# Kernel tuning notes

Measured on AMD Instinct MI355X. Metric: run time of the kernel, lower is better.

## Reference

```python
import jax, jax.numpy as jnp
import numpy as np
from jax import lax

B, N, M = 2, 16384, 4096
C1, C2 = 128, 256
H1, H2 = 256, 128  # mlp = [C1+C2, 256, 128]


def setup_inputs() -> dict:
    key = jax.random.key(0)
    ks = jax.random.split(key, 8)
    return {
        "unknown": jax.random.normal(ks[0], (B, N, 3), jnp.float32),
        "known": jax.random.normal(ks[1], (B, M, 3), jnp.float32),
        "unknow_feats": jax.random.normal(ks[2], (B, C1, N), jnp.float32),
        "known_feats": jax.random.normal(ks[3], (B, C2, M), jnp.float32),
        "W1": jax.random.normal(ks[4], (H1, C1 + C2), jnp.float32) * 0.05,
        "b1": jnp.zeros((H1,), jnp.float32),
        "W2": jax.random.normal(ks[5], (H2, H1), jnp.float32) * 0.05,
        "b2": jnp.zeros((H2,), jnp.float32),
    }


def reference(unknown, known, unknow_feats, known_feats, W1, b1, W2, b2):
    # Pairwise squared distances (B, n, m) via ||a||^2 + ||b||^2 - 2 a.b
    d2 = (
        jnp.sum(unknown * unknown, -1)[:, :, None]
        + jnp.sum(known * known, -1)[:, None, :]
        - 2.0 * jnp.einsum("bnd,bmd->bnm", unknown, known)
    )
    # 3 nearest neighbors
    neg_d2, idx = lax.top_k(-d2, 3)  # (B, n, 3)
    dist = jnp.sqrt(jnp.maximum(-neg_d2, 0.0))  # pointops returns sqrt distances
    dist_recip = 1.0 / (dist + 1e-8)
    weight = dist_recip / jnp.sum(dist_recip, axis=2, keepdims=True)  # (B, n, 3)
    # Gather neighbor features (B, C2, n, 3) and inverse-distance weighted sum
    gathered = jax.vmap(lambda f, i: f[:, i])(known_feats, idx)
    interpolated = jnp.sum(gathered * weight[:, None, :, :], axis=-1)  # (B, C2, n)
    new_features = jnp.concatenate([interpolated, unknow_feats], axis=1)  # (B, C1+C2, n)
    # Shared MLP (1x1 convs, bn=False -> conv bias + ReLU)
    h = jax.nn.relu(jnp.einsum("oc,bcn->bon", W1, new_features) + b1[None, :, None])
    out = jax.nn.relu(jnp.einsum("oc,bcn->bon", W2, h) + b2[None, :, None])
    return out  # (B, mlp[-1], n)
```

## Files before the change

### kernel.cpp

```cpp
#include <hip/hip_runtime.h>
#include <hip/hip_bf16.h>

#define BB 2
#define NN 16384
#define MM 4096
#define C1 128
#define C2 256
#define CIN 384
#define H1 256
#define H2 128
#define PT 32
#define XROW 392

typedef __attribute__((ext_vector_type(8))) short bf16x8;
typedef __attribute__((ext_vector_type(4))) float f32x4;
typedef __attribute__((ext_vector_type(2))) float f32x2;
typedef __attribute__((ext_vector_type(8))) float f32x8;

__device__ __forceinline__ short f32_to_bf16(float x) {
    unsigned u = __float_as_uint(x);
    u += 0x7fffu + ((u >> 16) & 1u);
    return (short)(u >> 16);
}
__device__ __forceinline__ float bf16_to_f32(unsigned short u) {
    union { unsigned u; float f; } c; c.u = ((unsigned)u) << 16; return c.f;
}
__device__ __forceinline__ unsigned pack_bf16x2(float a, float b) {
    __hip_bfloat162 h = __float22bfloat162_rn(make_float2(a, b));
    union { __hip_bfloat162 h; unsigned u; } cv;
    cv.h = h;
    return cv.u;
}

__global__ __launch_bounds__(1024) void kpk_prep_kernel(
    const float* __restrict__ known, float* __restrict__ kpk8)
{
    int i = blockIdx.x * 1024 + threadIdx.x;
    if (i < BB * MM) {
        float x = known[3 * i + 0], y = known[3 * i + 1], z = known[3 * i + 2];
        float n = fmaf(x, x, fmaf(y, y, z * z));
        int g = i >> 1, j = i & 1;
        float* base = kpk8 + (size_t)g * 8;
        base[0 + j] = x; base[2 + j] = y; base[4 + j] = z; base[6 + j] = n;
    }
}

__global__ __launch_bounds__(1024) void knn_aux_kernel(
    const float* __restrict__ unknown,
    const float* __restrict__ kpk8,
    int*   __restrict__ idx_out,
    float* __restrict__ w_out,
    const float* __restrict__ KF,
    unsigned short* __restrict__ KT16,
    const float* __restrict__ W1, const float* __restrict__ W2,
    short* __restrict__ W1b, short* __restrict__ W2b)
{
    __shared__ float pdv[16][64][3];
    __shared__ float vf[64];
    __shared__ float msc[64][8];
    __shared__ int   mid[64][8];
    __shared__ int   cnt[64];
    __shared__ float tl[32][33];

    const int bx  = blockIdx.x;
    const int tid = threadIdx.x;

    if (bx < 512) {
        const int lane = tid & 63;
        const int wv   = __builtin_amdgcn_readfirstlane(tid >> 6);
        const int b    = bx >> 8;
        const int n    = (bx & 255) * 64 + lane;

        if (tid < 64) cnt[tid] = 0;

        const float ux = unknown[((size_t)b * NN + n) * 3 + 0];
        const float uy = unknown[((size_t)b * NN + n) * 3 + 1];
        const float uz = unknown[((size_t)b * NN + n) * 3 + 2];
        const f32x2 ax2 = {-2.f * ux, -2.f * ux};
        const f32x2 ay2 = {-2.f * uy, -2.f * uy};
        const f32x2 az2 = {-2.f * uz, -2.f * uz};
        const float un = fmaf(ux, ux, fmaf(uy, uy, uz * uz));

        const int gbase = wv * 128;
        const float* __restrict__ kp = kpk8 + ((size_t)b * (MM / 2) + gbase) * 8;

        float v0 = 3e38f, v1 = 3e38f, v2 = 3e38f;
        #pragma unroll 4
        for (int g = 0; g < 128; ++g) {
            const f32x8 G = *(const f32x8*)(kp + (size_t)g * 8);
            const f32x2 kx = __builtin_shufflevector(G, G, 0, 1);
            const f32x2 ky = __builtin_shufflevector(G, G, 2, 3);
            const f32x2 kz = __builtin_shufflevector(G, G, 4, 5);
            const f32x2 kn = __builtin_shufflevector(G, G, 6, 7);
            const f32x2 sc2 = __builtin_elementwise_fma(ax2, kx,
                              __builtin_elementwise_fma(ay2, ky,
                              __builtin_elementwise_fma(az2, kz, kn)));
            float sa = sc2.x;
            v2 = __builtin_amdgcn_fmed3f(v1, sa, v2);
            v1 = __builtin_amdgcn_fmed3f(v0, sa, v1);
            v0 = fminf(sa, v0);
            float sb = sc2.y;
            v2 = __builtin_amdgcn_fmed3f(v1, sb, v2);
            v1 = __builtin_amdgcn_fmed3f(v0, sb, v1);
            v0 = fminf(sb, v0);
        }
        pdv[wv][lane][0] = v0; pdv[wv][lane][1] = v1; pdv[wv][lane][2] = v2;
        __syncthreads();

        if (tid < 64) {
            float r0 = 3e38f, r1 = 3e38f, r2 = 3e38f;
            #pragma unroll
            for (int ww = 0; ww < 16; ++ww) {
                #pragma unroll
                for (int k = 0; k < 3; ++k) {
                    float d = pdv[ww][tid][k];
                    r2 = __builtin_amdgcn_fmed3f(r1, d, r2);
                    r1 = __builtin_amdgcn_fmed3f(r0, d, r1);
                    r0 = fminf(d, r0);
                }
            }
            vf[tid] = r2;
        }
        __syncthreads();

        const float v2f = vf[lane];
        #pragma unroll 4
        for (int g = 0; g < 128; ++g) {
            const f32x8 G = *(const f32x8*)(kp + (size_t)g * 8);
            const f32x2 kx = __builtin_shufflevector(G, G, 0, 1);
            const f32x2 ky = __builtin_shufflevector(G, G, 2, 3);
            const f32x2 kz = __builtin_shufflevector(G, G, 4, 5);
            const f32x2 kn = __builtin_shufflevector(G, G, 6, 7);
            const f32x2 sc2 = __builtin_elementwise_fma(ax2, kx,
                              __builtin_elementwise_fma(ay2, ky,
                              __builtin_elementwise_fma(az2, kz, kn)));
            if (fminf(sc2.x, sc2.y) <= v2f) {
                if (sc2.x <= v2f) {
                    int c = atomicAdd(&cnt[lane], 1);
                    if (c < 8) { msc[lane][c] = sc2.x; mid[lane][c] = (gbase + g) * 2; }
                }
                if (sc2.y <= v2f) {
                    int c = atomicAdd(&cnt[lane], 1);
                    if (c < 8) { msc[lane][c] = sc2.y; mid[lane][c] = (gbase + g) * 2 + 1; }
                }
            }
        }
        __syncthreads();

        if (tid < 64) {
            const int c = cnt[tid] < 8 ? cnt[tid] : 8;
            float r0 = 3e38f, r1 = 3e38f, r2 = 3e38f;
            int   q0 = 0x7FFFFFFF, q1 = 0x7FFFFFFF, q2 = 0x7FFFFFFF;
            #pragma unroll
            for (int k = 0; k < 8; ++k) {
                float d = (k < c) ? msc[tid][k] : 3e38f;
                int   j = (k < c) ? mid[tid][k] : 0x7FFFFFFF;
                const bool lt0 = (d < r0) || (d == r0 && j < q0);
                const bool lt1 = (d < r1) || (d == r1 && j < q1);
                const bool lt2 = (d < r2) || (d == r2 && j < q2);
                float nr2 = lt1 ? r1 : (lt2 ? d : r2);
                int   nq2 = lt1 ? q1 : (lt2 ? j : q2);
                float nr1 = lt0 ? r0 : (lt1 ? d : r1);
                int   nq1 = lt0 ? q0 : (lt1 ? j : q1);
                float nr0 = lt0 ? d : r0;
                int   nq0 = lt0 ? j : q0;
                r0 = nr0; r1 = nr1; r2 = nr2; q0 = nq0; q1 = nq1; q2 = nq2;
            }
            float d0 = sqrtf(fmaxf(r0 + un, 0.f));
            float d1 = sqrtf(fmaxf(r1 + un, 0.f));
            float d2 = sqrtf(fmaxf(r2 + un, 0.f));
            float i0 = 1.f / (d0 + 1e-8f);
            float i1 = 1.f / (d1 + 1e-8f);
            float i2 = 1.f / (d2 + 1e-8f);
            float s  = i0 + i1 + i2;
            const size_t ob = ((size_t)(bx >> 8) * NN + n) * 3;
            idx_out[ob + 0] = q0; idx_out[ob + 1] = q1; idx_out[ob + 2] = q2;
            w_out[ob + 0] = i0 / s; w_out[ob + 1] = i1 / s; w_out[ob + 2] = i2 / s;
        }
    } else if (bx < 2560) {
        const int t  = bx - 512;
        const int b  = t >> 10;
        const int c0 = ((t >> 7) & 7) * 32;
        const int m0 = (t & 127) * 32;
        if (tid < 1024) {
            const int tx = tid & 31;
            const int ty = tid >> 5;
            tl[ty][tx] = KF[((size_t)b * C2 + c0 + ty) * MM + m0 + tx];
            __syncthreads();
            KT16[((size_t)b * MM + m0 + ty) * C2 + c0 + tx] = (unsigned short)f32_to_bf16(tl[tx][ty]);
        }
    } else {
        int i = (bx - 2560) * 1024 + tid;
        if (i < H1 * CIN) W1b[i] = f32_to_bf16(W1[i]);
        if (i < H2 * H1)  W2b[i] = f32_to_bf16(W2[i]);
    }
}

__global__ __launch_bounds__(256, 4) void fp_mlp_mfma_kernel(
    const float* __restrict__ unknow_feats,
    const unsigned short* __restrict__ KT16,
    const short* __restrict__ W1b,
    const float* __restrict__ b1,
    const short* __restrict__ W2b,
    const float* __restrict__ b2,
    const int*   __restrict__ idx,
    const float* __restrict__ wgt,
    float* __restrict__ out)
{
    __shared__ short XH[PT][XROW];
    __shared__ int   Is[PT * 3];
    __shared__ float Ws[PT * 3];

    const int tid  = threadIdx.x;
    const int blocks_per_b = NN / PT;
    const int b    = blockIdx.x / blocks_per_b;
    const int n0   = (blockIdx.x % blocks_per_b) * PT;
    const int w    = tid >> 6;
    const int lane = tid & 63;
    const int lr   = lane & 15;
    const int lq   = lane >> 4;

    if (tid < PT * 3) {
        const size_t base = ((size_t)b * NN + n0) * 3;
        Is[tid] = idx[base + tid];
        Ws[tid] = wgt[base + tid];
    }
    __syncthreads();

    {
        const unsigned short* KTb = KT16 + (size_t)b * MM * C2;
        const int c4 = (lane << 2);
        ushort4 g[8][3];
        #pragma unroll
        for (int i = 0; i < 8; ++i) {
            const int p = i * 4 + w;
            g[i][0] = *(const ushort4*)(KTb + (size_t)Is[3 * p + 0] * C2 + c4);
            g[i][1] = *(const ushort4*)(KTb + (size_t)Is[3 * p + 1] * C2 + c4);
            g[i][2] = *(const ushort4*)(KTb + (size_t)Is[3 * p + 2] * C2 + c4);
        }
        #pragma unroll
        for (int i = 0; i < 8; ++i) {
            const int p = i * 4 + w;
            const float w0 = Ws[3 * p + 0], w1 = Ws[3 * p + 1], w2 = Ws[3 * p + 2];
            float vx = fmaf(w0, bf16_to_f32(g[i][0].x), fmaf(w1, bf16_to_f32(g[i][1].x), w2 * bf16_to_f32(g[i][2].x)));
            float vy = fmaf(w0, bf16_to_f32(g[i][0].y), fmaf(w1, bf16_to_f32(g[i][1].y), w2 * bf16_to_f32(g[i][2].y)));
            float vz = fmaf(w0, bf16_to_f32(g[i][0].z), fmaf(w1, bf16_to_f32(g[i][1].z), w2 * bf16_to_f32(g[i][2].z)));
            float vw = fmaf(w0, bf16_to_f32(g[i][0].w), fmaf(w1, bf16_to_f32(g[i][1].w), w2 * bf16_to_f32(g[i][2].w)));
            uint2 pk;
            pk.x = pack_bf16x2(vx, vy);
            pk.y = pack_bf16x2(vz, vw);
            *(uint2*)&XH[p][c4] = pk;
        }
        const float* UFb = unknow_feats + (size_t)b * C1 * NN + n0;
        #pragma unroll
        for (int i = 0; i < 4; ++i) {
            int e  = i * 256 + tid;
            int cc = e >> 3;
            int nq = (e & 7) << 2;
            const float4 f = *(const float4*)(UFb + (size_t)cc * NN + nq);
            XH[nq + 0][C2 + cc] = f32_to_bf16(f.x);
            XH[nq + 1][C2 + cc] = f32_to_bf16(f.y);
            XH[nq + 2][C2 + cc] = f32_to_bf16(f.z);
            XH[nq + 3][C2 + cc] = f32_to_bf16(f.w);
        }
    }
    __syncthreads();

    f32x4 acc[4][2];
    #pragma unroll
    for (int t = 0; t < 4; ++t)
        #pragma unroll
        for (int p = 0; p < 2; ++p) acc[t][p] = (f32x4){0.f, 0.f, 0.f, 0.f};

    #pragma unroll 4
    for (int k0 = 0; k0 < CIN; k0 += 32) {
        bf16x8 a[4], x[2];
        #pragma unroll
        for (int t = 0; t < 4; ++t)
            a[t] = *(const bf16x8*)(W1b + (size_t)(w * 64 + t * 16 + lr) * CIN + k0 + lq * 8);
        #pragma unroll
        for (int p = 0; p < 2; ++p)
            x[p] = *(bf16x8*)&XH[p * 16 + lr][k0 + lq * 8];
        #pragma unroll
        for (int t = 0; t < 4; ++t)
            #pragma unroll
            for (int p = 0; p < 2; ++p)
                acc[t][p] = __builtin_amdgcn_mfma_f32_16x16x32_bf16(a[t], x[p], acc[t][p], 0, 0, 0);
    }
    __syncthreads();

    #pragma unroll
    for (int t = 0; t < 4; ++t) {
        const int obase = w * 64 + t * 16 + lq * 4;
        float bb0 = b1[obase + 0], bb1 = b1[obase + 1],
              bb2 = b1[obase + 2], bb3 = b1[obase + 3];
        #pragma unroll
        for (int p = 0; p < 2; ++p) {
            uint2 pk;
            pk.x = pack_bf16x2(fmaxf(acc[t][p].x + bb0, 0.f),
                               fmaxf(acc[t][p].y + bb1, 0.f));
            pk.y = pack_bf16x2(fmaxf(acc[t][p].z + bb2, 0.f),
                               fmaxf(acc[t][p].w + bb3, 0.f));
            *(uint2*)&XH[p * 16 + lr][obase] = pk;
        }
    }
    __syncthreads();

    {
        f32x4 acc2[2][2];
        #pragma unroll
        for (int t = 0; t < 2; ++t)
            #pragma unroll
            for (int p = 0; p < 2; ++p) acc2[t][p] = (f32x4){0.f, 0.f, 0.f, 0.f};

        #pragma unroll 4
        for (int k0 = 0; k0 < H1; k0 += 32) {
            bf16x8 a[2], h[2];
            #pragma unroll
            for (int t = 0; t < 2; ++t)
                a[t] = *(const bf16x8*)(W2b + (size_t)(w * 32 + t * 16 + lr) * H1 + k0 + lq * 8);
            #pragma unroll
            for (int p = 0; p < 2; ++p)
                h[p] = *(bf16x8*)&XH[p * 16 + lr][k0 + lq * 8];
            #pragma unroll
            for (int t = 0; t < 2; ++t)
                #pragma unroll
                for (int p = 0; p < 2; ++p)
                    acc2[t][p] = __builtin_amdgcn_mfma_f32_16x16x32_bf16(a[t], h[p], acc2[t][p], 0, 0, 0);
        }
        #pragma unroll
        for (int t = 0; t < 2; ++t) {
            const int obase = w * 32 + t * 16 + lq * 4;
            #pragma unroll
            for (int p = 0; p < 2; ++p) {
                const int n = n0 + p * 16 + lr;
                #pragma unroll
                for (int r = 0; r < 4; ++r) {
                    const int o = obase + r;
                    out[((size_t)b * H2 + o) * NN + n] =
                        fmaxf(((const float*)&acc2[t][p])[r] + b2[o], 0.f);
                }
            }
        }
    }
}

extern "C" void kernel_launch(void* const* d_in, const int* in_sizes, int n_in,
                              void* d_out, int out_size, void* d_ws, size_t ws_size,
                              hipStream_t stream) {
    const float* unknown      = (const float*)d_in[0];
    const float* known        = (const float*)d_in[1];
    const float* unknow_feats = (const float*)d_in[2];
    const float* known_feats  = (const float*)d_in[3];
    const float* W1           = (const float*)d_in[4];
    const float* b1           = (const float*)d_in[5];
    const float* W2           = (const float*)d_in[6];
    const float* b2           = (const float*)d_in[7];
    float* out = (float*)d_out;

    char* ws = (char*)d_ws;
    int*            idx  = (int*)(ws);
    float*          wgt  = (float*)(ws + 393216);
    short*          W1b  = (short*)(ws + 786432);
    short*          W2b  = (short*)(ws + 983040);
    float*          kpk8 = (float*)(ws + 1048576);
    unsigned short* KT16 = (unsigned short*)(ws + 1179648);

    kpk_prep_kernel<<<8, 1024, 0, stream>>>(known, kpk8);

    knn_aux_kernel<<<2656, 1024, 0, stream>>>(
        unknown, kpk8, idx, wgt, known_feats, KT16, W1, W2, W1b, W2b);

    fp_mlp_mfma_kernel<<<BB * (NN / PT), 256, 0, stream>>>(
        unknow_feats, KT16, W1b, b1, W2b, b2, idx, wgt, out);
}
```

Baseline: 166.2 us.

## Halve MLP point tile to 16, raise occupancy, split top-3 chains

Result: slower. 202.0 us (+21.5%).

```diff
diff --git a/kernel.cpp b/kernel.cpp
--- a/kernel.cpp
+++ b/kernel.cpp
@@ -9,7 +9,7 @@
 #define CIN 384
 #define H1 256
 #define H2 128
-#define PT 32
+#define PT 16
 #define XROW 392
 
 typedef __attribute__((ext_vector_type(8))) short bf16x8;
@@ -84,7 +84,8 @@
         const int gbase = wv * 128;
         const float* __restrict__ kp = kpk8 + ((size_t)b * (MM / 2) + gbase) * 8;
 
-        float v0 = 3e38f, v1 = 3e38f, v2 = 3e38f;
+        float va0 = 3e38f, va1 = 3e38f, va2 = 3e38f;
+        float vb0 = 3e38f, vb1 = 3e38f, vb2 = 3e38f;
         #pragma unroll 4
         for (int g = 0; g < 128; ++g) {
             const f32x8 G = *(const f32x8*)(kp + (size_t)g * 8);
@@ -96,15 +97,25 @@
                               __builtin_elementwise_fma(ay2, ky,
                               __builtin_elementwise_fma(az2, kz, kn)));
             float sa = sc2.x;
-            v2 = __builtin_amdgcn_fmed3f(v1, sa, v2);
-            v1 = __builtin_amdgcn_fmed3f(v0, sa, v1);
-            v0 = fminf(sa, v0);
+            va2 = __builtin_amdgcn_fmed3f(va1, sa, va2);
+            va1 = __builtin_amdgcn_fmed3f(va0, sa, va1);
+            va0 = fminf(sa, va0);
             float sb = sc2.y;
-            v2 = __builtin_amdgcn_fmed3f(v1, sb, v2);
-            v1 = __builtin_amdgcn_fmed3f(v0, sb, v1);
-            v0 = fminf(sb, v0);
-        }
-        pdv[wv][lane][0] = v0; pdv[wv][lane][1] = v1; pdv[wv][lane][2] = v2;
+            vb2 = __builtin_amdgcn_fmed3f(vb1, sb, vb2);
+            vb1 = __builtin_amdgcn_fmed3f(vb0, sb, vb1);
+            vb0 = fminf(sb, vb0);
+        }
+        {
+            float bv[3] = {vb0, vb1, vb2};
+            #pragma unroll
+            for (int k = 0; k < 3; ++k) {
+                float d = bv[k];
+                va2 = __builtin_amdgcn_fmed3f(va1, d, va2);
+                va1 = __builtin_amdgcn_fmed3f(va0, d, va1);
+                va0 = fminf(d, va0);
+            }
+        }
+        pdv[wv][lane][0] = va0; pdv[wv][lane][1] = va1; pdv[wv][lane][2] = va2;
         __syncthreads();
 
         if (tid < 64) {
@@ -182,7 +193,7 @@
         const int b  = t >> 10;
         const int c0 = ((t >> 7) & 7) * 32;
         const int m0 = (t & 127) * 32;
-        if (tid < 1024) {
+        {
             const int tx = tid & 31;
             const int ty = tid >> 5;
             tl[ty][tx] = KF[((size_t)b * C2 + c0 + ty) * MM + m0 + tx];
@@ -196,7 +207,7 @@
     }
 }
 
-__global__ __launch_bounds__(256, 4) void fp_mlp_mfma_kernel(
+__global__ __launch_bounds__(256, 7) void fp_mlp_mfma_kernel(
     const float* __restrict__ unknow_feats,
     const unsigned short* __restrict__ KT16,
     const short* __restrict__ W1b,
@@ -230,16 +241,16 @@
     {
         const unsigned short* KTb = KT16 + (size_t)b * MM * C2;
         const int c4 = (lane << 2);
-        ushort4 g[8][3];
-        #pragma unroll
-        for (int i = 0; i < 8; ++i) {
+        ushort4 g[4][3];
+        #pragma unroll
+        for (int i = 0; i < 4; ++i) {
             const int p = i * 4 + w;
             g[i][0] = *(const ushort4*)(KTb + (size_t)Is[3 * p + 0] * C2 + c4);
             g[i][1] = *(const ushort4*)(KTb + (size_t)Is[3 * p + 1] * C2 + c4);
             g[i][2] = *(const ushort4*)(KTb + (size_t)Is[3 * p + 2] * C2 + c4);
         }
         #pragma unroll
-        for (int i = 0; i < 8; ++i) {
+        for (int i = 0; i < 4; ++i) {
             const int p = i * 4 + w;
             const float w0 = Ws[3 * p + 0], w1 = Ws[3 * p + 1], w2 = Ws[3 * p + 2];
             float vx = fmaf(w0, bf16_to_f32(g[i][0].x), fmaf(w1, bf16_to_f32(g[i][1].x), w2 * bf16_to_f32(g[i][2].x)));
@@ -253,10 +264,10 @@
         }
         const float* UFb = unknow_feats + (size_t)b * C1 * NN + n0;
         #pragma unroll
-        for (int i = 0; i < 4; ++i) {
+        for (int i = 0; i < 2; ++i) {
             int e  = i * 256 + tid;
-            int cc = e >> 3;
-            int nq = (e & 7) << 2;
+            int cc = e >> 2;
+            int nq = (e & 3) << 2;
             const float4 f = *(const float4*)(UFb + (size_t)cc * NN + nq);
             XH[nq + 0][C2 + cc] = f32_to_bf16(f.x);
             XH[nq + 1][C2 + cc] = f32_to_bf16(f.y);
@@ -266,26 +277,20 @@
     }
     __syncthreads();
 
-    f32x4 acc[4][2];
+    f32x4 acc[4];
     #pragma unroll
-    for (int t = 0; t < 4; ++t)
-        #pragma unroll
-        for (int p = 0; p < 2; ++p) acc[t][p] = (f32x4){0.f, 0.f, 0.f, 0.f};
+    for (int t = 0; t < 4; ++t) acc[t] = (f32x4){0.f, 0.f, 0.f, 0.f};
 
     #pragma unroll 4
     for (int k0 = 0; k0 < CIN; k0 += 32) {
-        bf16x8 a[4], x[2];
+        bf16x8 a[4], x;
         #pragma unroll
         for (int t = 0; t < 4; ++t)
             a[t] = *(const bf16x8*)(W1b + (size_t)(w * 64 + t * 16 + lr) * CIN + k0 + lq * 8);
-        #pragma unroll
-        for (int p = 0; p < 2; ++p)
-            x[p] = *(bf16x8*)&XH[p * 16 + lr][k0 + lq * 8];
+        x = *(bf16x8*)&XH[lr][k0 + lq * 8];
         #pragma unroll
         for (int t = 0; t < 4; ++t)
-            #pragma unroll
-            for (int p = 0; p < 2; ++p)
-                acc[t][p] = __builtin_amdgcn_mfma_f32_16x16x32_bf16(a[t], x[p], acc[t][p], 0, 0, 0);
+            acc[t] = __builtin_amdgcn_mfma_f32_16x16x32_bf16(a[t], x, acc[t], 0, 0, 0);
     }
     __syncthreads();
 
@@ -294,52 +299,40 @@
         const int obase = w * 64 + t * 16 + lq * 4;
         float bb0 = b1[obase + 0], bb1 = b1[obase + 1],
               bb2 = b1[obase + 2], bb3 = b1[obase + 3];
-        #pragma unroll
-        for (int p = 0; p < 2; ++p) {
-            uint2 pk;
-            pk.x = pack_bf16x2(fmaxf(acc[t][p].x + bb0, 0.f),
-                               fmaxf(acc[t][p].y + bb1, 0.f));
-            pk.y = pack_bf16x2(fmaxf(acc[t][p].z + bb2, 0.f),
-                               fmaxf(acc[t][p].w + bb3, 0.f));
-            *(uint2*)&XH[p * 16 + lr][obase] = pk;
-        }
+        uint2 pk;
+        pk.x = pack_bf16x2(fmaxf(acc[t].x + bb0, 0.f),
+                           fmaxf(acc[t].y + bb1, 0.f));
+        pk.y = pack_bf16x2(fmaxf(acc[t].z + bb2, 0.f),
+                           fmaxf(acc[t].w + bb3, 0.f));
+        *(uint2*)&XH[lr][obase] = pk;
     }
     __syncthreads();
 
     {
-        f32x4 acc2[2][2];
-        #pragma unroll
-        for (int t = 0; t < 2; ++t)
-            #pragma unroll
-            for (int p = 0; p < 2; ++p) acc2[t][p] = (f32x4){0.f, 0.f, 0.f, 0.f};
+        f32x4 acc2[2];
+        #pragma unroll
+        for (int t = 0; t < 2; ++t) acc2[t] = (f32x4){0.f, 0.f, 0.f, 0.f};
 
         #pragma unroll 4
         for (int k0 = 0; k0 < H1; k0 += 32) {
-            bf16x8 a[2], h[2];
+            bf16x8 a[2], h;
             #pragma unroll
             for (int t = 0; t < 2; ++t)
                 a[t] = *(const bf16x8*)(W2b + (size_t)(w * 32 + t * 16 + lr) * H1 + k0 + lq * 8);
-            #pragma unroll
-            for (int p = 0; p < 2; ++p)
-                h[p] = *(bf16x8*)&XH[p * 16 + lr][k0 + lq * 8];
+            h = *(bf16x8*)&XH[lr][k0 + lq * 8];
             #pragma unroll
             for (int t = 0; t < 2; ++t)
-                #pragma unroll
-                for (int p = 0; p < 2; ++p)
-                    acc2[t][p] = __builtin_amdgcn_mfma_f32_16x16x32_bf16(a[t], h[p], acc2[t][p], 0, 0, 0);
+                acc2[t] = __builtin_amdgcn_mfma_f32_16x16x32_bf16(a[t], h, acc2[t], 0, 0, 0);
         }
         #pragma unroll
         for (int t = 0; t < 2; ++t) {
             const int obase = w * 32 + t * 16 + lq * 4;
-            #pragma unroll
-            for (int p = 0; p < 2; ++p) {
-                const int n = n0 + p * 16 + lr;
-                #pragma unroll
-                for (int r = 0; r < 4; ++r) {
-                    const int o = obase + r;
-                    out[((size_t)b * H2 + o) * NN + n] =
-                        fmaxf(((const float*)&acc2[t][p])[r] + b2[o], 0.f);
-                }
+            const int n = n0 + lr;
+            #pragma unroll
+            for (int r = 0; r < 4; ++r) {
+                const int o = obase + r;
+                out[((size_t)b * H2 + o) * NN + n] =
+                    fmaxf(((const float*)&acc2[t])[r] + b2[o], 0.f);
             }
         }
     }
```

## Process two point tiles per MLP block with prefetched gathers; split kNN chains

Applied to the files above, without the earlier changes.

New measurement: 167.9 us. Within noise of the previous version (+1.0%).

```diff
diff --git a/kernel.cpp b/kernel.cpp
--- a/kernel.cpp
+++ b/kernel.cpp
@@ -10,6 +10,7 @@
 #define H1 256
 #define H2 128
 #define PT 32
+#define TILES 2
 #define XROW 392
 
 typedef __attribute__((ext_vector_type(8))) short bf16x8;
@@ -84,7 +85,8 @@
         const int gbase = wv * 128;
         const float* __restrict__ kp = kpk8 + ((size_t)b * (MM / 2) + gbase) * 8;
 
-        float v0 = 3e38f, v1 = 3e38f, v2 = 3e38f;
+        float va0 = 3e38f, va1 = 3e38f, va2 = 3e38f;
+        float vb0 = 3e38f, vb1 = 3e38f, vb2 = 3e38f;
         #pragma unroll 4
         for (int g = 0; g < 128; ++g) {
             const f32x8 G = *(const f32x8*)(kp + (size_t)g * 8);
@@ -96,15 +98,25 @@
                               __builtin_elementwise_fma(ay2, ky,
                               __builtin_elementwise_fma(az2, kz, kn)));
             float sa = sc2.x;
-            v2 = __builtin_amdgcn_fmed3f(v1, sa, v2);
-            v1 = __builtin_amdgcn_fmed3f(v0, sa, v1);
-            v0 = fminf(sa, v0);
+            va2 = __builtin_amdgcn_fmed3f(va1, sa, va2);
+            va1 = __builtin_amdgcn_fmed3f(va0, sa, va1);
+            va0 = fminf(sa, va0);
             float sb = sc2.y;
-            v2 = __builtin_amdgcn_fmed3f(v1, sb, v2);
-            v1 = __builtin_amdgcn_fmed3f(v0, sb, v1);
-            v0 = fminf(sb, v0);
-        }
-        pdv[wv][lane][0] = v0; pdv[wv][lane][1] = v1; pdv[wv][lane][2] = v2;
+            vb2 = __builtin_amdgcn_fmed3f(vb1, sb, vb2);
+            vb1 = __builtin_amdgcn_fmed3f(vb0, sb, vb1);
+            vb0 = fminf(sb, vb0);
+        }
+        {
+            float bv[3] = {vb0, vb1, vb2};
+            #pragma unroll
+            for (int k = 0; k < 3; ++k) {
+                float d = bv[k];
+                va2 = __builtin_amdgcn_fmed3f(va1, d, va2);
+                va1 = __builtin_amdgcn_fmed3f(va0, d, va1);
+                va0 = fminf(d, va0);
+            }
+        }
+        pdv[wv][lane][0] = va0; pdv[wv][lane][1] = va1; pdv[wv][lane][2] = va2;
         __syncthreads();
 
         if (tid < 64) {
@@ -182,7 +194,7 @@
         const int b  = t >> 10;
         const int c0 = ((t >> 7) & 7) * 32;
         const int m0 = (t & 127) * 32;
-        if (tid < 1024) {
+        {
             const int tx = tid & 31;
             const int ty = tid >> 5;
             tl[ty][tx] = KF[((size_t)b * C2 + c0 + ty) * MM + m0 + tx];
@@ -196,7 +208,7 @@
     }
 }
 
-__global__ __launch_bounds__(256, 4) void fp_mlp_mfma_kernel(
+__global__ __launch_bounds__(256) void fp_mlp_mfma_kernel(
     const float* __restrict__ unknow_feats,
     const unsigned short* __restrict__ KT16,
     const short* __restrict__ W1b,
@@ -208,40 +220,42 @@
     float* __restrict__ out)
 {
     __shared__ short XH[PT][XROW];
-    __shared__ int   Is[PT * 3];
-    __shared__ float Ws[PT * 3];
+    __shared__ int   Is[TILES][PT * 3];
+    __shared__ float Ws[TILES][PT * 3];
 
     const int tid  = threadIdx.x;
-    const int blocks_per_b = NN / PT;
-    const int b    = blockIdx.x / blocks_per_b;
-    const int n0   = (blockIdx.x % blocks_per_b) * PT;
+    const int blk  = blockIdx.x;
+    const int b    = blk >> 8;
+    const int t0   = (blk & 255) * TILES;
     const int w    = tid >> 6;
     const int lane = tid & 63;
     const int lr   = lane & 15;
     const int lq   = lane >> 4;
-
-    if (tid < PT * 3) {
-        const size_t base = ((size_t)b * NN + n0) * 3;
-        Is[tid] = idx[base + tid];
-        Ws[tid] = wgt[base + tid];
+    const int c4   = lane << 2;
+
+    if (tid < TILES * PT * 3) {
+        const int tt = tid / (PT * 3), e = tid % (PT * 3);
+        const size_t base = ((size_t)b * NN + (size_t)(t0 + tt) * PT) * 3;
+        Is[tt][e] = idx[base + e];
+        Ws[tt][e] = wgt[base + e];
     }
     __syncthreads();
 
+    const unsigned short* KTb = KT16 + (size_t)b * MM * C2;
+
+    ushort4 g[8][3];
+    #pragma unroll
+    for (int i = 0; i < 8; ++i) {
+        const int p = i * 4 + w;
+        g[i][0] = *(const ushort4*)(KTb + (size_t)Is[0][3 * p + 0] * C2 + c4);
+        g[i][1] = *(const ushort4*)(KTb + (size_t)Is[0][3 * p + 1] * C2 + c4);
+        g[i][2] = *(const ushort4*)(KTb + (size_t)Is[0][3 * p + 2] * C2 + c4);
+    }
     {
-        const unsigned short* KTb = KT16 + (size_t)b * MM * C2;
-        const int c4 = (lane << 2);
-        ushort4 g[8][3];
         #pragma unroll
         for (int i = 0; i < 8; ++i) {
             const int p = i * 4 + w;
-            g[i][0] = *(const ushort4*)(KTb + (size_t)Is[3 * p + 0] * C2 + c4);
-            g[i][1] = *(const ushort4*)(KTb + (size_t)Is[3 * p + 1] * C2 + c4);
-            g[i][2] = *(const ushort4*)(KTb + (size_t)Is[3 * p + 2] * C2 + c4);
-        }
-        #pragma unroll
-        for (int i = 0; i < 8; ++i) {
-            const int p = i * 4 + w;
-            const float w0 = Ws[3 * p + 0], w1 = Ws[3 * p + 1], w2 = Ws[3 * p + 2];
+            const float w0 = Ws[0][3 * p + 0], w1 = Ws[0][3 * p + 1], w2 = Ws[0][3 * p + 2];
             float vx = fmaf(w0, bf16_to_f32(g[i][0].x), fmaf(w1, bf16_to_f32(g[i][1].x), w2 * bf16_to_f32(g[i][2].x)));
             float vy = fmaf(w0, bf16_to_f32(g[i][0].y), fmaf(w1, bf16_to_f32(g[i][1].y), w2 * bf16_to_f32(g[i][2].y)));
             float vz = fmaf(w0, bf16_to_f32(g[i][0].z), fmaf(w1, bf16_to_f32(g[i][1].z), w2 * bf16_to_f32(g[i][2].z)));
@@ -251,7 +265,7 @@
             pk.y = pack_bf16x2(vz, vw);
             *(uint2*)&XH[p][c4] = pk;
         }
-        const float* UFb = unknow_feats + (size_t)b * C1 * NN + n0;
+        const float* UFb = unknow_feats + (size_t)b * C1 * NN + (size_t)t0 * PT;
         #pragma unroll
         for (int i = 0; i < 4; ++i) {
             int e  = i * 256 + tid;
@@ -266,81 +280,125 @@
     }
     __syncthreads();
 
-    f32x4 acc[4][2];
-    #pragma unroll
-    for (int t = 0; t < 4; ++t)
+    for (int t = 0; t < TILES; ++t) {
+        const int n0 = (t0 + t) * PT;
+
+        if (t + 1 < TILES) {
+            #pragma unroll
+            for (int i = 0; i < 8; ++i) {
+                const int p = i * 4 + w;
+                g[i][0] = *(const ushort4*)(KTb + (size_t)Is[t + 1][3 * p + 0] * C2 + c4);
+                g[i][1] = *(const ushort4*)(KTb + (size_t)Is[t + 1][3 * p + 1] * C2 + c4);
+                g[i][2] = *(const ushort4*)(KTb + (size_t)Is[t + 1][3 * p + 2] * C2 + c4);
+            }
+        }
+
+        f32x4 acc[4][2];
         #pragma unroll
-        for (int p = 0; p < 2; ++p) acc[t][p] = (f32x4){0.f, 0.f, 0.f, 0.f};
-
-    #pragma unroll 4
-    for (int k0 = 0; k0 < CIN; k0 += 32) {
-        bf16x8 a[4], x[2];
+        for (int tt = 0; tt < 4; ++tt)
+            #pragma unroll
+            for (int p = 0; p < 2; ++p) acc[tt][p] = (f32x4){0.f, 0.f, 0.f, 0.f};
+
+        #pragma unroll 4
+        for (int k0 = 0; k0 < CIN; k0 += 32) {
+            bf16x8 a[4], x[2];
+            #pragma unroll
+            for (int tt = 0; tt < 4; ++tt)
+                a[tt] = *(const bf16x8*)(W1b + (size_t)(w * 64 + tt * 16 + lr) * CIN + k0 + lq * 8);
+            #pragma unroll
+            for (int p = 0; p < 2; ++p)
+                x[p] = *(bf16x8*)&XH[p * 16 + lr][k0 + lq * 8];
+            #pragma unroll
+            for (int tt = 0; tt < 4; ++tt)
+                #pragma unroll
+                for (int p = 0; p < 2; ++p)
+                    acc[tt][p] = __builtin_amdgcn_mfma_f32_16x16x32_bf16(a[tt], x[p], acc[tt][p], 0, 0, 0);
+        }
+        __syncthreads();
+
         #pragma unroll
-        for (int t = 0; t < 4; ++t)
-            a[t] = *(const bf16x8*)(W1b + (size_t)(w * 64 + t * 16 + lr) * CIN + k0 + lq * 8);
-        #pragma unroll
-        for (int p = 0; p < 2; ++p)
-            x[p] = *(bf16x8*)&XH[p * 16 + lr][k0 + lq * 8];
-        #pragma unroll
-        for (int t = 0; t < 4; ++t)
-            #pragma unroll
-            for (int p = 0; p < 2; ++p)
-                acc[t][p] = __builtin_amdgcn_mfma_f32_16x16x32_bf16(a[t], x[p], acc[t][p], 0, 0, 0);
-    }
-    __syncthreads();
-
-    #pragma unroll
-    for (int t = 0; t < 4; ++t) {
-        const int obase = w * 64 + t * 16 + lq * 4;
-        float bb0 = b1[obase + 0], bb1 = b1[obase + 1],
-              bb2 = b1[obase + 2], bb3 = b1[obase + 3];
-        #pragma unroll
-        for (int p = 0; p < 2; ++p) {
-            uint2 pk;
-            pk.x = pack_bf16x2(fmaxf(acc[t][p].x + bb0, 0.f),
-                               fmaxf(acc[t][p].y + bb1, 0.f));
-            pk.y = pack_bf16x2(fmaxf(acc[t][p].z + bb2, 0.f),
-                               fmaxf(acc[t][p].w + bb3, 0.f));
-            *(uint2*)&XH[p * 16 + lr][obase] = pk;
-        }
-    }
-    __syncthreads();
-
-    {
-        f32x4 acc2[2][2];
-        #pragma unroll
-        for (int t = 0; t < 2; ++t)
-            #pragma unroll
-            for (int p = 0; p < 2; ++p) acc2[t][p] = (f32x4){0.f, 0.f, 0.f, 0.f};
-
-        #pragma unroll 4
-        for (int k0 = 0; k0 < H1; k0 += 32) {
-            bf16x8 a[2], h[2];
-            #pragma unroll
-            for (int t = 0; t < 2; ++t)
-                a[t] = *(const bf16x8*)(W2b + (size_t)(w * 32 + t * 16 + lr) * H1 + k0 + lq * 8);
-            #pragma unroll
-            for (int p = 0; p < 2; ++p)
-                h[p] = *(bf16x8*)&XH[p * 16 + lr][k0 + lq * 8];
-            #pragma unroll
-            for (int t = 0; t < 2; ++t)
+        for (int tt = 0; tt < 4; ++tt) {
+            const int obase = w * 64 + tt * 16 + lq * 4;
+            float bb0 = b1[obase + 0], bb1 = b1[obase + 1],
+                  bb2 = b1[obase + 2], bb3 = b1[obase + 3];
+            #pragma unroll
+            for (int p = 0; p < 2; ++p) {
+                uint2 pk;
+                pk.x = pack_bf16x2(fmaxf(acc[tt][p].x + bb0, 0.f),
+                                   fmaxf(acc[tt][p].y + bb1, 0.f));
+                pk.y = pack_bf16x2(fmaxf(acc[tt][p].z + bb2, 0.f),
+                                   fmaxf(acc[tt][p].w + bb3, 0.f));
+                *(uint2*)&XH[p * 16 + lr][obase] = pk;
+            }
+        }
+        __syncthreads();
+
+        {
+            f32x4 acc2[2][2];
+            #pragma unroll
+            for (int tt = 0; tt < 2; ++tt)
+                #pragma unroll
+                for (int p = 0; p < 2; ++p) acc2[tt][p] = (f32x4){0.f, 0.f, 0.f, 0.f};
+
+            #pragma unroll 4
+            for (int k0 = 0; k0 < H1; k0 += 32) {
+                bf16x8 a[2], h[2];
+                #pragma unroll
+                for (int tt = 0; tt < 2; ++tt)
+                    a[tt] = *(const bf16x8*)(W2b + (size_t)(w * 32 + tt * 16 + lr) * H1 + k0 + lq * 8);
                 #pragma unroll
                 for (int p = 0; p < 2; ++p)
-                    acc2[t][p] = __builtin_amdgcn_mfma_f32_16x16x32_bf16(a[t], h[p], acc2[t][p], 0, 0, 0);
-        }
-        #pragma unroll
-        for (int t = 0; t < 2; ++t) {
-            const int obase = w * 32 + t * 16 + lq * 4;
-            #pragma unroll
-            for (int p = 0; p < 2; ++p) {
-                const int n = n0 + p * 16 + lr;
-                #pragma unroll
-                for (int r = 0; r < 4; ++r) {
-                    const int o = obase + r;
-                    out[((size_t)b * H2 + o) * NN + n] =
-                        fmaxf(((const float*)&acc2[t][p])[r] + b2[o], 0.f);
+                    h[p] = *(bf16x8*)&XH[p * 16 + lr][k0 + lq * 8];
+                #pragma unroll
+                for (int tt = 0; tt < 2; ++tt)
+                    #pragma unroll
+                    for (int p = 0; p < 2; ++p)
+                        acc2[tt][p] = __builtin_amdgcn_mfma_f32_16x16x32_bf16(a[tt], h[p], acc2[tt][p], 0, 0, 0);
+            }
+            #pragma unroll
+            for (int tt = 0; tt < 2; ++tt) {
+                const int obase = w * 32 + tt * 16 + lq * 4;
+                #pragma unroll
+                for (int p = 0; p < 2; ++p) {
+                    const int n = n0 + p * 16 + lr;
+                    #pragma unroll
+                    for (int r = 0; r < 4; ++r) {
+                        const int o = obase + r;
+                        out[((size_t)b * H2 + o) * NN + n] =
+                            fmaxf(((const float*)&acc2[tt][p])[r] + b2[o], 0.f);
+                    }
                 }
             }
+        }
+        __syncthreads();
+
+        if (t + 1 < TILES) {
+            #pragma unroll
+            for (int i = 0; i < 8; ++i) {
+                const int p = i * 4 + w;
+                const float w0 = Ws[t + 1][3 * p + 0], w1 = Ws[t + 1][3 * p + 1], w2 = Ws[t + 1][3 * p + 2];
+                float vx = fmaf(w0, bf16_to_f32(g[i][0].x), fmaf(w1, bf16_to_f32(g[i][1].x), w2 * bf16_to_f32(g[i][2].x)));
+                float vy = fmaf(w0, bf16_to_f32(g[i][0].y), fmaf(w1, bf16_to_f32(g[i][1].y), w2 * bf16_to_f32(g[i][2].y)));
+                float vz = fmaf(w0, bf16_to_f32(g[i][0].z), fmaf(w1, bf16_to_f32(g[i][1].z), w2 * bf16_to_f32(g[i][2].z)));
+                float vw = fmaf(w0, bf16_to_f32(g[i][0].w), fmaf(w1, bf16_to_f32(g[i][1].w), w2 * bf16_to_f32(g[i][2].w)));
+                uint2 pk;
+                pk.x = pack_bf16x2(vx, vy);
+                pk.y = pack_bf16x2(vz, vw);
+                *(uint2*)&XH[p][c4] = pk;
+            }
+            const float* UFb = unknow_feats + (size_t)b * C1 * NN + (size_t)(t0 + t + 1) * PT;
+            #pragma unroll
+            for (int i = 0; i < 4; ++i) {
+                int e  = i * 256 + tid;
+                int cc = e >> 3;
+                int nq = (e & 7) << 2;
+                const float4 f = *(const float4*)(UFb + (size_t)cc * NN + nq);
+                XH[nq + 0][C2 + cc] = f32_to_bf16(f.x);
+                XH[nq + 1][C2 + cc] = f32_to_bf16(f.y);
+                XH[nq + 2][C2 + cc] = f32_to_bf16(f.z);
+                XH[nq + 3][C2 + cc] = f32_to_bf16(f.w);
+            }
+            __syncthreads();
         }
     }
 }
@@ -371,6 +429,6 @@
     knn_aux_kernel<<<2656, 1024, 0, stream>>>(
         unknown, kpk8, idx, wgt, known_feats, KT16, W1, W2, W1b, W2b);
 
-    fp_mlp_mfma_kernel<<<BB * (NN / PT), 256, 0, stream>>>(
+    fp_mlp_mfma_kernel<<<BB * NN / (PT * TILES), 256, 0, stream>>>(
         unknow_feats, KT16, W1b, b1, W2b, b2, idx, wgt, out);
 }
```
